# Kernel optimization log

Hardware: AMD Instinct MI355X
Metric: run time of the kernel (lower is better)

Reference implementation:

```python
import jax, jax.numpy as jnp
import numpy as np

B, T, IN, OUT = 4, 2048, 4096, 11008


def setup_inputs() -> dict:
    key = jax.random.key(0)
    k1, k2, k3, k4 = jax.random.split(key, 4)
    x = jax.random.normal(k1, (B, T, IN), dtype=jnp.float32)
    # int8 weight values in [-127, 127]; stored as int32 for harness dtype support
    weight_int8 = jax.random.randint(k2, (OUT, IN), -127, 128, dtype=jnp.int32)
    # per-output-channel scales, positive and small like absmax/127
    weight_scale = jax.random.uniform(k3, (OUT, 1), dtype=jnp.float32, minval=1e-4, maxval=0.02)
    bias = jax.random.normal(k4, (OUT,), dtype=jnp.float32) * 0.01
    return {"x": x, "weight_int8": weight_int8, "weight_scale": weight_scale, "bias": bias}


def reference(x, weight_int8, weight_scale, bias):
    # dequantize: [OUT, IN] float weight = int8 * per-row scale
    weight_fp = weight_int8.astype(jnp.float32) * weight_scale
    weight_fp = weight_fp.astype(x.dtype)
    # F.linear: x @ W^T + b -> [B, T, OUT]
    out = jnp.einsum('bti,oi->bto', x, weight_fp) + bias
    return out
```

## Files before the change

kernel.cpp:

```cpp
#include <hip/hip_runtime.h>
#include <hip/hip_bf16.h>

#define MDIM 8192
#define NDIM 11008
#define KDIM 4096

#define BM 256
#define BN 256
#define BK 64
#define NT (KDIM / BK)

typedef __attribute__((ext_vector_type(4))) int   int4v;
typedef __attribute__((ext_vector_type(4))) float f32x4;


__global__ __launch_bounds__(256) void quant_x_kernel(const float* __restrict__ x,
                                                      int* __restrict__ q,
                                                      float* __restrict__ xs) {
  int row = blockIdx.x;
  int tid = threadIdx.x;
  const float4* xr = (const float4*)(x + (size_t)row * KDIM);
  float4 v[4];
  float amax = 0.f;
#pragma unroll
  for (int i = 0; i < 4; ++i) {
    v[i] = xr[tid + i * 256];
    amax = fmaxf(amax, fmaxf(fmaxf(fabsf(v[i].x), fabsf(v[i].y)),
                             fmaxf(fabsf(v[i].z), fabsf(v[i].w))));
  }
#pragma unroll
  for (int off = 32; off; off >>= 1)
    amax = fmaxf(amax, __shfl_xor(amax, off));
  __shared__ float smax[4];
  if ((tid & 63) == 0) smax[tid >> 6] = amax;
  __syncthreads();
  amax = fmaxf(fmaxf(smax[0], smax[1]), fmaxf(smax[2], smax[3]));
  amax = fmaxf(amax, 1e-20f);
  float inv = 127.f / amax;
  if (tid == 0) xs[row] = amax * (1.f / 127.f);
  int* qr = q + (size_t)row * (KDIM / 4);
#pragma unroll
  for (int i = 0; i < 4; ++i) {
    int a = (int)rintf(v[i].x * inv) & 255;
    int b = (int)rintf(v[i].y * inv) & 255;
    int c = (int)rintf(v[i].z * inv) & 255;
    int d = (int)rintf(v[i].w * inv);
    qr[tid + i * 256] = a | (b << 8) | (c << 16) | (d << 24);
  }
}


__global__ void cvt_w_kernel(const int* __restrict__ w, int* __restrict__ q, int n) {
  int stride = gridDim.x * blockDim.x;
  for (int i = blockIdx.x * blockDim.x + threadIdx.x; i < n; i += stride) {
    int4v v = *(const int4v*)(w + (size_t)i * 4);
    q[i] = (v.x & 255) | ((v.y & 255) << 8) | ((v.z & 255) << 16) | (v.w << 24);
  }
}


#define SBARR() __builtin_amdgcn_sched_barrier(0)
#define BARR()  __builtin_amdgcn_s_barrier()
#define VMW_(n) asm volatile("s_waitcnt vmcnt(" #n ")" ::: "memory")
#define VMW(n)  VMW_(n)

#define GLL(SRC, DST) \
  __builtin_amdgcn_global_load_lds( \
      (const __attribute__((address_space(1))) void*)(SRC), \
      (__attribute__((address_space(3))) void*)(DST), 16, 0, 0)

#define STAGE(GSRC, LBASE, BUFI, T) do { \
    const char* _s = (GSRC) + (T) * 64; \
    GLL(_s, (LBASE) + (BUFI) * 16384 + w * 1024); \
    GLL(_s + rstep, (LBASE) + (BUFI) * 16384 + w * 1024 + 8192); \
  } while (0)

#define RD(LB, BUFI, ROW) \
  (*(const int4v*)((LB) + (BUFI) * 16384 + (ROW) * 64 + kbs))

#define MFMA16(AF, MOFF) do { \
    _Pragma("unroll") for (int mi = 0; mi < 4; ++mi) \
    _Pragma("unroll") for (int ni = 0; ni < 4; ++ni) \
      acc[(MOFF) + mi][ni] = __builtin_amdgcn_mfma_i32_16x16x64_i8( \
          af[mi], bf[ni], acc[(MOFF) + mi][ni], 0, 0, 0); \
  } while (0)

#define KT(T, B_, SD, VN, TAIL) do { \
    _Pragma("unroll") for (int ni = 0; ni < 4; ++ni) bf[ni] = RD(ldsB, B_, brow0 + ni * 16); \
    _Pragma("unroll") for (int mi = 0; mi < 4; ++mi) af[mi] = RD(ldsA, B_, arow0 + mi * 16); \
    if (SD) STAGE(gAs, ldsA, ((B_) + 2) & 3, (T) + 2); \
    SBARR(); \
    __builtin_amdgcn_s_setprio(1); MFMA16(af, 0); __builtin_amdgcn_s_setprio(0); \
    SBARR(); \
    _Pragma("unroll") for (int mi = 0; mi < 4; ++mi) af[mi] = RD(ldsA, B_, arow0 + 64 + mi * 16); \
    if (SD) STAGE(gBs, ldsB, ((B_) + 2) & 3, (T) + 2); \
    SBARR(); \
    __builtin_amdgcn_s_setprio(1); MFMA16(af, 4); __builtin_amdgcn_s_setprio(0); \
    SBARR(); \
    if (!(TAIL)) { VMW(VN); BARR(); SBARR(); } \
  } while (0)

__global__ __launch_bounds__(512, 2) void gemm_i8_kernel(
    const char* __restrict__ A,
    const char* __restrict__ Bt,
    const float* __restrict__ xs,
    const float* __restrict__ scale,
    const float* __restrict__ bias,
    float* __restrict__ C)
{
  __shared__ __attribute__((aligned(16))) char As[4][256][64];
  __shared__ __attribute__((aligned(16))) char Bs[4][256][64];

  const int nbc = NDIM / BN;
  int bid = blockIdx.x;
  int cpx = gridDim.x >> 3;
  int swz = (bid & 7) * cpx + (bid >> 3);
  int brow = (swz / nbc) * BM;
  int bcol = (swz % nbc) * BN;

  int tid  = threadIdx.x;
  int lane = tid & 63;
  int w    = tid >> 6;
  int wr   = (w >> 2) & 1;
  int wc   = w & 3;

  int ra = lane & 15;
  int kb = (lane >> 4) * 16;
  int kbs = kb ^ (((ra >> 1) & 3) << 4);

  int arow0 = wr * 128 + ra;
  int brow0 = wc * 64 + ra;

  int srow = w * 16 + (lane >> 2);
  int csrc = (lane & 3) ^ ((lane >> 3) & 3);
  const char* gAs = A  + (size_t)(brow + srow) * KDIM + csrc * 16;
  const char* gBs = Bt + (size_t)(bcol + srow) * KDIM + csrc * 16;
  const size_t rstep = (size_t)128 * KDIM;

  char* ldsA = &As[0][0][0];
  char* ldsB = &Bs[0][0][0];

  int4v acc[8][4] = {};
  int4v af[4], bf[4];

  STAGE(gAs, ldsA, 0, 0);  STAGE(gBs, ldsB, 0, 0);
  STAGE(gAs, ldsA, 1, 1);  STAGE(gBs, ldsB, 1, 1);
  VMW(4); BARR(); SBARR();

  for (int t = 0; t < 56; t += 4) {
    KT(t,     0, 1, 4, 0);
    KT(t + 1, 1, 1, 4, 0);
    KT(t + 2, 2, 1, 4, 0);
    KT(t + 3, 3, 1, 4, 0);
  }
  KT(56, 0, 1, 4, 0);
  KT(57, 1, 1, 4, 0);
  KT(58, 2, 1, 4, 0);
  KT(59, 3, 1, 4, 0);
  KT(60, 0, 1, 4, 0);
  KT(61, 1, 1, 4, 0);
  KT(62, 2, 0, 0, 0);
  KT(63, 3, 0, 0, 1);

  int col0 = bcol + wc * 64 + ra;
  int row0 = brow + wr * 128 + (lane >> 4) * 4;
  float xr_[8][4];
#pragma unroll
  for (int m = 0; m < 8; ++m)
#pragma unroll
    for (int j = 0; j < 4; ++j)
      xr_[m][j] = xs[row0 - brow + brow + m * 16 + j];
#pragma unroll
  for (int n = 0; n < 4; ++n) {
    int ng = col0 + n * 16;
    float sc = scale[ng];
    float bi = bias[ng];
#pragma unroll
    for (int m = 0; m < 8; ++m) {
      int rg = row0 + m * 16;
#pragma unroll
      for (int j = 0; j < 4; ++j)
        C[(size_t)(rg + j) * NDIM + ng] = (float)acc[m][n][j] * (xr_[m][j] * sc) + bi;
    }
  }
}


__global__ void naive_kernel(const float* __restrict__ x, const int* __restrict__ w,
                             const float* __restrict__ scale, const float* __restrict__ bias,
                             float* __restrict__ out)
{
  int n = blockIdx.x * blockDim.x + threadIdx.x;
  int m = blockIdx.y;
  if (n >= NDIM) return;
  const float* xr = x + (size_t)m * KDIM;
  const int* wrow = w + (size_t)n * KDIM;
  float s = 0.f;
  for (int k = 0; k < KDIM; ++k) s += xr[k] * (float)wrow[k];
  out[(size_t)m * NDIM + n] = s * scale[n] + bias[n];
}


extern "C" void kernel_launch(void* const* d_in, const int* in_sizes, int n_in,
                              void* d_out, int out_size, void* d_ws, size_t ws_size,
                              hipStream_t stream) {
  const float* x      = (const float*)d_in[0];
  const int*   w8     = (const int*)d_in[1];
  const float* wscale = (const float*)d_in[2];
  const float* bias   = (const float*)d_in[3];
  float* out = (float*)d_out;

  size_t aq = (size_t)MDIM * KDIM;
  size_t bq = (size_t)NDIM * KDIM;
  size_t xb = (size_t)MDIM * 4;

  if (ws_size >= aq + bq + xb) {
    char* Aq = (char*)d_ws;
    char* Bq = (char*)d_ws + aq;
    float* xsp = (float*)((char*)d_ws + aq + bq);
    quant_x_kernel<<<MDIM, 256, 0, stream>>>(x, (int*)Aq, xsp);
    cvt_w_kernel<<<2048, 256, 0, stream>>>(w8, (int*)Bq, NDIM * KDIM / 4);
    gemm_i8_kernel<<<(MDIM / BM) * (NDIM / BN), 512, 0, stream>>>(
        Aq, Bq, xsp, wscale, bias, out);
  } else {
    naive_kernel<<<dim3((NDIM + 255) / 256, MDIM), 256, 0, stream>>>(x, w8, wscale, bias, out);
  }
}
```

Baseline: 506.1 us.

## Switch int8 GEMM to 32x32x32 MFMA with register double-buffered LDS reads

Replaces the 16x16x64 int8 MFMA tiling with 32x32x32 MFMAs (8 accumulators of 16 ints per wave) and changes the LDS swizzle to match the new fragment layout. Deepens the global-to-LDS prefetch from 2 to 3 tiles ahead and double-buffers the A/B fragments in registers, so LDS reads for the next k-slice overlap the current MFMA batch. The epilogue is rewritten for the 32x32 output layout and uses nontemporal stores. The larger MFMA needs fewer LDS fragment reads per FLOP, but register pressure rises at 2 waves/SIMD, and the new swizzle and stage indexing must stay consistent.

```diff
diff --git a/kernel.cpp b/kernel.cpp
--- a/kernel.cpp
+++ b/kernel.cpp
@@ -10,8 +10,8 @@
 #define BK 64
 #define NT (KDIM / BK)
 
-typedef __attribute__((ext_vector_type(4))) int   int4v;
-typedef __attribute__((ext_vector_type(4))) float f32x4;
+typedef __attribute__((ext_vector_type(4)))  int   int4v;
+typedef __attribute__((ext_vector_type(16))) int   int16v;
 
 
 __global__ __launch_bounds__(256) void quant_x_kernel(const float* __restrict__ x,
@@ -75,29 +75,32 @@
     GLL(_s + rstep, (LBASE) + (BUFI) * 16384 + w * 1024 + 8192); \
   } while (0)
 
-#define RD(LB, BUFI, ROW) \
-  (*(const int4v*)((LB) + (BUFI) * 16384 + (ROW) * 64 + kbs))
-
-#define MFMA16(AF, MOFF) do { \
-    _Pragma("unroll") for (int mi = 0; mi < 4; ++mi) \
-    _Pragma("unroll") for (int ni = 0; ni < 4; ++ni) \
-      acc[(MOFF) + mi][ni] = __builtin_amdgcn_mfma_i32_16x16x64_i8( \
-          af[mi], bf[ni], acc[(MOFF) + mi][ni], 0, 0, 0); \
+#define RD32(LB, SLOT, RBASE, KB) \
+  (*(const int4v*)((LB) + (SLOT) * 16384 + ((RBASE) + ln31) * 64 + (KB)))
+
+#define CL(AA, BB) do { \
+    _Pragma("unroll") for (int mt = 0; mt < 4; ++mt) \
+    _Pragma("unroll") for (int nt = 0; nt < 2; ++nt) \
+      acc[mt * 2 + nt] = __builtin_amdgcn_mfma_i32_32x32x32_i8( \
+          AA[mt], BB[nt], acc[mt * 2 + nt], 0, 0, 0); \
   } while (0)
 
-#define KT(T, B_, SD, VN, TAIL) do { \
-    _Pragma("unroll") for (int ni = 0; ni < 4; ++ni) bf[ni] = RD(ldsB, B_, brow0 + ni * 16); \
-    _Pragma("unroll") for (int mi = 0; mi < 4; ++mi) af[mi] = RD(ldsA, B_, arow0 + mi * 16); \
-    if (SD) STAGE(gAs, ldsA, ((B_) + 2) & 3, (T) + 2); \
-    SBARR(); \
-    __builtin_amdgcn_s_setprio(1); MFMA16(af, 0); __builtin_amdgcn_s_setprio(0); \
-    SBARR(); \
-    _Pragma("unroll") for (int mi = 0; mi < 4; ++mi) af[mi] = RD(ldsA, B_, arow0 + 64 + mi * 16); \
-    if (SD) STAGE(gBs, ldsB, ((B_) + 2) & 3, (T) + 2); \
-    SBARR(); \
-    __builtin_amdgcn_s_setprio(1); MFMA16(af, 4); __builtin_amdgcn_s_setprio(0); \
-    SBARR(); \
-    if (!(TAIL)) { VMW(VN); BARR(); SBARR(); } \
+#define KT(T, SLT, SD, EN, PF, LASTT) do { \
+    _Pragma("unroll") for (int mt = 0; mt < 4; ++mt) aS1[mt] = RD32(ldsA, SLT, arow + mt * 32, koff1); \
+    _Pragma("unroll") for (int nt = 0; nt < 2; ++nt) bS1[nt] = RD32(ldsB, SLT, bcolr + nt * 32, koff1); \
+    if (SD) STAGE(gAs, ldsA, ((SLT) + 3) & 3, (T) + 3); \
+    SBARR(); \
+    __builtin_amdgcn_s_setprio(1); CL(aS0, bS0); __builtin_amdgcn_s_setprio(0); \
+    SBARR(); \
+    if (PF) { \
+      _Pragma("unroll") for (int mt = 0; mt < 4; ++mt) aS0[mt] = RD32(ldsA, ((SLT) + 1) & 3, arow + mt * 32, koff0); \
+      _Pragma("unroll") for (int nt = 0; nt < 2; ++nt) bS0[nt] = RD32(ldsB, ((SLT) + 1) & 3, bcolr + nt * 32, koff0); \
+    } \
+    if (SD) STAGE(gBs, ldsB, ((SLT) + 3) & 3, (T) + 3); \
+    SBARR(); \
+    __builtin_amdgcn_s_setprio(1); CL(aS1, bS1); __builtin_amdgcn_s_setprio(0); \
+    SBARR(); \
+    if (!(LASTT)) { VMW(EN); BARR(); SBARR(); } \
   } while (0)
 
 __global__ __launch_bounds__(512, 2) void gemm_i8_kernel(
@@ -124,15 +127,18 @@
   int wr   = (w >> 2) & 1;
   int wc   = w & 3;
 
-  int ra = lane & 15;
-  int kb = (lane >> 4) * 16;
-  int kbs = kb ^ (((ra >> 1) & 3) << 4);
-
-  int arow0 = wr * 128 + ra;
-  int brow0 = wc * 64 + ra;
-
+  int ln31 = lane & 31;
+  int hi   = lane >> 5;
+  int keyl  = ((lane >> 1) & 3) ^ ((lane >> 3) & 3);
+  int koff0 = ((hi ^ keyl) << 4);
+  int koff1 = koff0 ^ 32;
+
+  int arow  = wr * 128;
+  int bcolr = wc * 64;
+
+  int srow_key = ((lane >> 3) & 3) ^ ((2 * w + (lane >> 5)) & 3);
+  int csrc = (lane & 3) ^ srow_key;
   int srow = w * 16 + (lane >> 2);
-  int csrc = (lane & 3) ^ ((lane >> 3) & 3);
   const char* gAs = A  + (size_t)(brow + srow) * KDIM + csrc * 16;
   const char* gBs = Bt + (size_t)(bcol + srow) * KDIM + csrc * 16;
   const size_t rstep = (size_t)128 * KDIM;
@@ -140,47 +146,45 @@
   char* ldsA = &As[0][0][0];
   char* ldsB = &Bs[0][0][0];
 
-  int4v acc[8][4] = {};
-  int4v af[4], bf[4];
+  int16v acc[8] = {};
+  int4v aS0[4], bS0[2], aS1[4], bS1[2];
 
   STAGE(gAs, ldsA, 0, 0);  STAGE(gBs, ldsB, 0, 0);
   STAGE(gAs, ldsA, 1, 1);  STAGE(gBs, ldsB, 1, 1);
+  STAGE(gAs, ldsA, 2, 2);  STAGE(gBs, ldsB, 2, 2);
   VMW(4); BARR(); SBARR();
 
-  for (int t = 0; t < 56; t += 4) {
-    KT(t,     0, 1, 4, 0);
-    KT(t + 1, 1, 1, 4, 0);
-    KT(t + 2, 2, 1, 4, 0);
-    KT(t + 3, 3, 1, 4, 0);
-  }
-  KT(56, 0, 1, 4, 0);
-  KT(57, 1, 1, 4, 0);
-  KT(58, 2, 1, 4, 0);
-  KT(59, 3, 1, 4, 0);
-  KT(60, 0, 1, 4, 0);
-  KT(61, 1, 1, 4, 0);
-  KT(62, 2, 0, 0, 0);
-  KT(63, 3, 0, 0, 1);
-
-  int col0 = bcol + wc * 64 + ra;
-  int row0 = brow + wr * 128 + (lane >> 4) * 4;
-  float xr_[8][4];
-#pragma unroll
-  for (int m = 0; m < 8; ++m)
-#pragma unroll
-    for (int j = 0; j < 4; ++j)
-      xr_[m][j] = xs[row0 - brow + brow + m * 16 + j];
-#pragma unroll
-  for (int n = 0; n < 4; ++n) {
-    int ng = col0 + n * 16;
-    float sc = scale[ng];
-    float bi = bias[ng];
-#pragma unroll
-    for (int m = 0; m < 8; ++m) {
-      int rg = row0 + m * 16;
-#pragma unroll
-      for (int j = 0; j < 4; ++j)
-        C[(size_t)(rg + j) * NDIM + ng] = (float)acc[m][n][j] * (xr_[m][j] * sc) + bi;
+#pragma unroll
+  for (int mt = 0; mt < 4; ++mt) aS0[mt] = RD32(ldsA, 0, arow + mt * 32, koff0);
+#pragma unroll
+  for (int nt = 0; nt < 2; ++nt) bS0[nt] = RD32(ldsB, 0, bcolr + nt * 32, koff0);
+
+  for (int t = 0; t < 60; t += 4) {
+    KT(t,     0, 1, 4, 1, 0);
+    KT(t + 1, 1, 1, 4, 1, 0);
+    KT(t + 2, 2, 1, 4, 1, 0);
+    KT(t + 3, 3, 1, 4, 1, 0);
+  }
+  KT(60, 0, 1, 4, 1, 0);
+  KT(61, 1, 0, 0, 1, 0);
+  KT(62, 2, 0, 0, 1, 0);
+  KT(63, 3, 0, 0, 0, 1);
+
+  int col0  = bcol + wc * 64 + ln31;
+  int rbase = brow + wr * 128 + 4 * hi;
+#pragma unroll
+  for (int mt = 0; mt < 4; ++mt) {
+#pragma unroll
+    for (int r = 0; r < 16; ++r) {
+      int rg = rbase + mt * 32 + (r & 3) + 8 * (r >> 2);
+      float xv = xs[rg];
+#pragma unroll
+      for (int nt = 0; nt < 2; ++nt) {
+        int ng = col0 + nt * 32;
+        __builtin_nontemporal_store(
+            (float)acc[mt * 2 + nt][r] * (xv * scale[ng]) + bias[ng],
+            &C[(size_t)rg * NDIM + ng]);
+      }
     }
   }
 }
```

Result: no change. 501.3 us (-1.0%).
